# Kernel tuning notes

Hardware: AMD Instinct MI355X
Metric: run time of the kernel (lower is better)

The kernel has to match this reference:

```python
import jax, jax.numpy as jnp
import numpy as np

K_SIZE = 5  # local window size (odd, SAME padding, stride 1)


def _local_attn(x_main, x_ref, W_main, W_ref, k_size=K_SIZE):
    # 1x1 convs == per-pixel channel matmuls
    cm = jnp.einsum('bhwc,cd->bhwd', x_main, W_main)  # query  [B,H,W,C']
    cr = jnp.einsum('bhwc,cd->bhwd', x_ref, W_ref)    # keys   [B,H,W,C']
    pad = (k_size - 1) // 2
    B, H, W, C = cr.shape
    crp = jnp.pad(cr, ((0, 0), (pad, pad), (pad, pad), (0, 0)))
    # score for each of the k*k offsets: dot(query, shifted key) per pixel.
    # Avoids materializing the [B,H,W,k*k,C] patch tensor.
    scores = [
        jnp.einsum('bhwc,bhwc->bhw', cm, crp[:, i:i + H, j:j + W, :])
        for i in range(k_size) for j in range(k_size)
    ]
    # the layer concatenates the query itself as the last "key" (self score)
    scores.append(jnp.einsum('bhwc,bhwc->bhw', cm, cm))
    attn = jnp.stack(scores, axis=-1)  # [B,H,W,k*k+1]
    return jax.nn.softmax(attn, axis=-1)


def setup_inputs() -> dict:
    key = jax.random.key(0)
    k1, k2, k3, k4 = jax.random.split(key, 4)
    B, H, W, C = 4, 128, 128, 64
    Ci = 64  # intermediate_dim
    return {
        'x_main': jax.random.normal(k1, (B, H, W, C), jnp.float32),
        'x_ref': jax.random.normal(k2, (B, H, W, C), jnp.float32),
        'W_main': jax.random.normal(k3, (C, Ci), jnp.float32) * (2.0 / C) ** 0.5,
        'W_ref': jax.random.normal(k4, (C, Ci), jnp.float32) * (2.0 / C) ** 0.5,
    }


def reference(x_main, x_ref, W_main, W_ref):
    return _local_attn(x_main, x_ref, W_main, W_ref)
```

## Files before the change

### kernel.cpp

```cpp
#include <hip/hip_runtime.h>
#include <math.h>

#define HDIM 128
#define WDIM 128
#define CDIM 64
#define BDIM 4

#define TILE_W 16
#define TILE_H 8
#define HALO_W 20
#define HALO_H 12
#define NHALO (HALO_W * HALO_H)
#define PSTRIDE 68
#define WSTRIDE 65

typedef short bf16x8 __attribute__((ext_vector_type(8)));
typedef float f32x4  __attribute__((ext_vector_type(4)));

__device__ __forceinline__ void split_bf16(float f, short& hi, short& lo) {
    unsigned u = __float_as_uint(f);
    hi = (short)(u >> 16);
    float hf = __uint_as_float(u & 0xffff0000u);
    float l  = f - hf;
    lo = (short)(__float_as_uint(l) >> 16);
}

__global__ __launch_bounds__(256, 1)
void fused_mfma_local_attn(const float* __restrict__ xm,
                           const float* __restrict__ xr,
                           const float* __restrict__ Wm,
                           const float* __restrict__ Wr,
                           float* __restrict__ out) {
    __shared__ float lds[16320];
    float* Wsh = lds;
    float* cms = lds + 4352;
    float* crs = lds;

    const int t    = threadIdx.x;
    const int lane = t & 63;
    const int wv   = t >> 6;
    const int m    = lane & 15;
    const int quad = lane >> 4;
    const int tx0  = blockIdx.x * TILE_W;
    const int ty0  = blockIdx.y * TILE_H;
    const int b    = blockIdx.z;

    #pragma unroll
    for (int i = 0; i < 16; ++i) {
        int L = t + 256 * i;
        Wsh[(L >> 6) * WSTRIDE + (L & 63)] = Wm[L];
    }
    __syncthreads();

    bf16x8 Bhi[2][4], Blo[2][4];
    #pragma unroll
    for (int ks = 0; ks < 2; ++ks)
        #pragma unroll
        for (int nt = 0; nt < 4; ++nt)
            #pragma unroll
            for (int j = 0; j < 8; ++j) {
                float f = Wsh[(ks * 32 + quad * 8 + j) * WSTRIDE + nt * 16 + m];
                short hi, lo; split_bf16(f, hi, lo);
                Bhi[ks][nt][j] = hi; Blo[ks][nt][j] = lo;
            }

    #pragma unroll
    for (int s = 0; s < 2; ++s) {
        const int tile = 2 * wv + s;
        const float* ap = xm + (((size_t)b * HDIM + ty0 + tile) * WDIM
                                + tx0 + m) * CDIM + quad * 8;
        float4 p0 = *(const float4*)(ap);
        float4 p1 = *(const float4*)(ap + 4);
        float4 p2 = *(const float4*)(ap + 32);
        float4 p3 = *(const float4*)(ap + 36);

        bf16x8 Ahi[2], Alo[2];
        {
            float fv[16] = {p0.x,p0.y,p0.z,p0.w, p1.x,p1.y,p1.z,p1.w,
                            p2.x,p2.y,p2.z,p2.w, p3.x,p3.y,p3.z,p3.w};
            #pragma unroll
            for (int ks = 0; ks < 2; ++ks)
                #pragma unroll
                for (int j = 0; j < 8; ++j) {
                    short hi, lo; split_bf16(fv[8 * ks + j], hi, lo);
                    Ahi[ks][j] = hi; Alo[ks][j] = lo;
                }
        }
        f32x4 acc[4];
        #pragma unroll
        for (int nt = 0; nt < 4; ++nt)
            { acc[nt][0]=0.f; acc[nt][1]=0.f; acc[nt][2]=0.f; acc[nt][3]=0.f; }
        #pragma unroll
        for (int ks = 0; ks < 2; ++ks)
            #pragma unroll
            for (int nt = 0; nt < 4; ++nt) {
                acc[nt] = __builtin_amdgcn_mfma_f32_16x16x32_bf16(Ahi[ks], Bhi[ks][nt], acc[nt], 0,0,0);
                acc[nt] = __builtin_amdgcn_mfma_f32_16x16x32_bf16(Ahi[ks], Blo[ks][nt], acc[nt], 0,0,0);
                acc[nt] = __builtin_amdgcn_mfma_f32_16x16x32_bf16(Alo[ks], Bhi[ks][nt], acc[nt], 0,0,0);
            }
        #pragma unroll
        for (int nt = 0; nt < 4; ++nt)
            #pragma unroll
            for (int r = 0; r < 4; ++r)
                cms[(tile * 16 + quad * 4 + r) * PSTRIDE + nt * 16 + m] = acc[nt][r];
    }
    __syncthreads();

    #pragma unroll
    for (int i = 0; i < 16; ++i) {
        int L = t + 256 * i;
        Wsh[(L >> 6) * WSTRIDE + (L & 63)] = Wr[L];
    }
    __syncthreads();

    #pragma unroll
    for (int ks = 0; ks < 2; ++ks)
        #pragma unroll
        for (int nt = 0; nt < 4; ++nt)
            #pragma unroll
            for (int j = 0; j < 8; ++j) {
                float f = Wsh[(ks * 32 + quad * 8 + j) * WSTRIDE + nt * 16 + m];
                short hi, lo; split_bf16(f, hi, lo);
                Bhi[ks][nt][j] = hi; Blo[ks][nt][j] = lo;
            }

    const int pl = t >> 1;
    const int cg = t & 1;
    float4 qv[8];
    #pragma unroll
    for (int mq = 0; mq < 8; ++mq)
        qv[mq] = *(const float4*)&cms[pl * PSTRIDE + cg * 32 + 4 * mq];
    __syncthreads();

    #pragma unroll
    for (int s = 0; s < 4; ++s) {
        const int tj = wv + 4 * s;
        if (tj < 15) {
            const int hp = tj * 16 + m;
            const int hy = hp / HALO_W;
            const int hx = hp - hy * HALO_W;
            const int gy = ty0 + hy - 2, gx = tx0 + hx - 2;
            float4 p0 = make_float4(0,0,0,0), p1 = p0, p2 = p0, p3 = p0;
            if (gy >= 0 && gy < HDIM && gx >= 0 && gx < WDIM) {
                const float* ap = xr + (((size_t)b * HDIM + gy) * WDIM + gx) * CDIM
                                  + quad * 8;
                p0 = *(const float4*)(ap);
                p1 = *(const float4*)(ap + 4);
                p2 = *(const float4*)(ap + 32);
                p3 = *(const float4*)(ap + 36);
            }
            bf16x8 Ahi[2], Alo[2];
            {
                float fv[16] = {p0.x,p0.y,p0.z,p0.w, p1.x,p1.y,p1.z,p1.w,
                                p2.x,p2.y,p2.z,p2.w, p3.x,p3.y,p3.z,p3.w};
                #pragma unroll
                for (int ks = 0; ks < 2; ++ks)
                    #pragma unroll
                    for (int j = 0; j < 8; ++j) {
                        short hi, lo; split_bf16(fv[8 * ks + j], hi, lo);
                        Ahi[ks][j] = hi; Alo[ks][j] = lo;
                    }
            }
            f32x4 acc[4];
            #pragma unroll
            for (int nt = 0; nt < 4; ++nt)
                { acc[nt][0]=0.f; acc[nt][1]=0.f; acc[nt][2]=0.f; acc[nt][3]=0.f; }
            #pragma unroll
            for (int ks = 0; ks < 2; ++ks)
                #pragma unroll
                for (int nt = 0; nt < 4; ++nt) {
                    acc[nt] = __builtin_amdgcn_mfma_f32_16x16x32_bf16(Ahi[ks], Bhi[ks][nt], acc[nt], 0,0,0);
                    acc[nt] = __builtin_amdgcn_mfma_f32_16x16x32_bf16(Ahi[ks], Blo[ks][nt], acc[nt], 0,0,0);
                    acc[nt] = __builtin_amdgcn_mfma_f32_16x16x32_bf16(Alo[ks], Bhi[ks][nt], acc[nt], 0,0,0);
                }
            #pragma unroll
            for (int nt = 0; nt < 4; ++nt)
                #pragma unroll
                for (int r = 0; r < 4; ++r)
                    crs[(tj * 16 + quad * 4 + r) * PSTRIDE + nt * 16 + m] = acc[nt][r];
        }
    }
    __syncthreads();

    const int lx = pl & (TILE_W - 1);
    const int ly = pl >> 4;
    const size_t gpx = ((size_t)b * HDIM + ty0 + ly) * WDIM + tx0 + lx;

    float s[26];
    #pragma unroll
    for (int k = 0; k < 25; ++k) {
        const int i = k / 5, j = k % 5;
        const int p = (ly + i) * HALO_W + (lx + j);
        const float4* kp = (const float4*)&crs[p * PSTRIDE + cg * 32];
        float acc = 0.f;
        #pragma unroll
        for (int mq = 0; mq < 8; ++mq) {
            float4 v = kp[mq];
            acc = fmaf(qv[mq].x, v.x, acc);
            acc = fmaf(qv[mq].y, v.y, acc);
            acc = fmaf(qv[mq].z, v.z, acc);
            acc = fmaf(qv[mq].w, v.w, acc);
        }
        s[k] = acc;
    }
    {
        float acc = 0.f;
        #pragma unroll
        for (int mq = 0; mq < 8; ++mq) {
            float4 v = qv[mq];
            acc = fmaf(v.x, v.x, acc);
            acc = fmaf(v.y, v.y, acc);
            acc = fmaf(v.z, v.z, acc);
            acc = fmaf(v.w, v.w, acc);
        }
        s[25] = acc;
    }

    #pragma unroll
    for (int k = 0; k < 26; ++k) s[k] += __shfl_xor(s[k], 1);

    float mx = s[0];
    #pragma unroll
    for (int k = 1; k < 26; ++k) mx = fmaxf(mx, s[k]);
    float sum = 0.f;
    #pragma unroll
    for (int k = 0; k < 26; ++k) { s[k] = __expf(s[k] - mx); sum += s[k]; }
    const float inv = 1.f / sum;

    float* op = &out[gpx * 26 + cg * 13];
    if (cg == 0) {
        #pragma unroll
        for (int k = 0; k < 13; ++k) op[k] = s[k] * inv;
    } else {
        #pragma unroll
        for (int k = 0; k < 13; ++k) op[k] = s[13 + k] * inv;
    }
}

extern "C" void kernel_launch(void* const* d_in, const int* in_sizes, int n_in,
                              void* d_out, int out_size, void* d_ws, size_t ws_size,
                              hipStream_t stream) {
    const float* xm = (const float*)d_in[0];
    const float* xr = (const float*)d_in[1];
    const float* Wm = (const float*)d_in[2];
    const float* Wr = (const float*)d_in[3];
    float* outp = (float*)d_out;

    dim3 g(WDIM / TILE_W, HDIM / TILE_H, BDIM);
    fused_mfma_local_attn<<<g, 256, 0, stream>>>(xm, xr, Wm, Wr, outp);
}
```

Measured before the change: 89.44 us.

## Split fused kernel into projection kernel and score/softmax kernel via workspace

Splits the fused kernel into two. The first projects both x_main and x_ref to global workspace buffers using split-bf16 MFMA, with no halo recomputation. The second loads the projected key halo and the queries from the workspace and computes the 26 scores and the softmax. This removes the redundant projection of halo pixels (12x20 per 8x16 tile) and the serialized phases within one block. In exchange it adds a global round trip of about 32 MB of intermediates and a second kernel launch.

```diff
diff --git a/kernel.cpp b/kernel.cpp
--- a/kernel.cpp
+++ b/kernel.cpp
@@ -10,7 +10,7 @@
 #define TILE_H 8
 #define HALO_W 20
 #define HALO_H 12
-#define NHALO (HALO_W * HALO_H)
+#define NPX (HALO_W * HALO_H)
 #define PSTRIDE 68
 #define WSTRIDE 65
 
@@ -25,16 +25,12 @@
     lo = (short)(__float_as_uint(l) >> 16);
 }
 
+
 __global__ __launch_bounds__(256, 1)
-void fused_mfma_local_attn(const float* __restrict__ xm,
-                           const float* __restrict__ xr,
-                           const float* __restrict__ Wm,
-                           const float* __restrict__ Wr,
-                           float* __restrict__ out) {
-    __shared__ float lds[16320];
-    float* Wsh = lds;
-    float* cms = lds + 4352;
-    float* crs = lds;
+void k1_proj(const float* __restrict__ xm, const float* __restrict__ xr,
+             const float* __restrict__ Wm, const float* __restrict__ Wr,
+             float* __restrict__ cm, float* __restrict__ cr) {
+    __shared__ float Wsh[2][64 * WSTRIDE];
 
     const int t    = threadIdx.x;
     const int lane = t & 63;
@@ -48,107 +44,39 @@
     #pragma unroll
     for (int i = 0; i < 16; ++i) {
         int L = t + 256 * i;
-        Wsh[(L >> 6) * WSTRIDE + (L & 63)] = Wm[L];
+        int r = L >> 6, c = L & 63;
+        Wsh[0][r * WSTRIDE + c] = Wm[L];
+        Wsh[1][r * WSTRIDE + c] = Wr[L];
     }
     __syncthreads();
 
-    bf16x8 Bhi[2][4], Blo[2][4];
-    #pragma unroll
-    for (int ks = 0; ks < 2; ++ks)
-        #pragma unroll
-        for (int nt = 0; nt < 4; ++nt)
-            #pragma unroll
-            for (int j = 0; j < 8; ++j) {
-                float f = Wsh[(ks * 32 + quad * 8 + j) * WSTRIDE + nt * 16 + m];
-                short hi, lo; split_bf16(f, hi, lo);
-                Bhi[ks][nt][j] = hi; Blo[ks][nt][j] = lo;
-            }
-
-    #pragma unroll
-    for (int s = 0; s < 2; ++s) {
-        const int tile = 2 * wv + s;
-        const float* ap = xm + (((size_t)b * HDIM + ty0 + tile) * WDIM
-                                + tx0 + m) * CDIM + quad * 8;
-        float4 p0 = *(const float4*)(ap);
-        float4 p1 = *(const float4*)(ap + 4);
-        float4 p2 = *(const float4*)(ap + 32);
-        float4 p3 = *(const float4*)(ap + 36);
-
-        bf16x8 Ahi[2], Alo[2];
-        {
-            float fv[16] = {p0.x,p0.y,p0.z,p0.w, p1.x,p1.y,p1.z,p1.w,
-                            p2.x,p2.y,p2.z,p2.w, p3.x,p3.y,p3.z,p3.w};
-            #pragma unroll
-            for (int ks = 0; ks < 2; ++ks)
+    #pragma unroll 1
+    for (int w = 0; w < 2; ++w) {
+        const float* __restrict__ src = w ? xr : xm;
+        float* __restrict__ dst       = w ? cr : cm;
+
+        bf16x8 Bhi[2][4], Blo[2][4];
+        #pragma unroll
+        for (int ks = 0; ks < 2; ++ks)
+            #pragma unroll
+            for (int nt = 0; nt < 4; ++nt)
                 #pragma unroll
                 for (int j = 0; j < 8; ++j) {
-                    short hi, lo; split_bf16(fv[8 * ks + j], hi, lo);
-                    Ahi[ks][j] = hi; Alo[ks][j] = lo;
+                    float f = Wsh[w][(ks * 32 + quad * 8 + j) * WSTRIDE + nt * 16 + m];
+                    short hi, lo; split_bf16(f, hi, lo);
+                    Bhi[ks][nt][j] = hi; Blo[ks][nt][j] = lo;
                 }
-        }
-        f32x4 acc[4];
-        #pragma unroll
-        for (int nt = 0; nt < 4; ++nt)
-            { acc[nt][0]=0.f; acc[nt][1]=0.f; acc[nt][2]=0.f; acc[nt][3]=0.f; }
-        #pragma unroll
-        for (int ks = 0; ks < 2; ++ks)
-            #pragma unroll
-            for (int nt = 0; nt < 4; ++nt) {
-                acc[nt] = __builtin_amdgcn_mfma_f32_16x16x32_bf16(Ahi[ks], Bhi[ks][nt], acc[nt], 0,0,0);
-                acc[nt] = __builtin_amdgcn_mfma_f32_16x16x32_bf16(Ahi[ks], Blo[ks][nt], acc[nt], 0,0,0);
-                acc[nt] = __builtin_amdgcn_mfma_f32_16x16x32_bf16(Alo[ks], Bhi[ks][nt], acc[nt], 0,0,0);
-            }
-        #pragma unroll
-        for (int nt = 0; nt < 4; ++nt)
-            #pragma unroll
-            for (int r = 0; r < 4; ++r)
-                cms[(tile * 16 + quad * 4 + r) * PSTRIDE + nt * 16 + m] = acc[nt][r];
-    }
-    __syncthreads();
-
-    #pragma unroll
-    for (int i = 0; i < 16; ++i) {
-        int L = t + 256 * i;
-        Wsh[(L >> 6) * WSTRIDE + (L & 63)] = Wr[L];
-    }
-    __syncthreads();
-
-    #pragma unroll
-    for (int ks = 0; ks < 2; ++ks)
-        #pragma unroll
-        for (int nt = 0; nt < 4; ++nt)
-            #pragma unroll
-            for (int j = 0; j < 8; ++j) {
-                float f = Wsh[(ks * 32 + quad * 8 + j) * WSTRIDE + nt * 16 + m];
-                short hi, lo; split_bf16(f, hi, lo);
-                Bhi[ks][nt][j] = hi; Blo[ks][nt][j] = lo;
-            }
-
-    const int pl = t >> 1;
-    const int cg = t & 1;
-    float4 qv[8];
-    #pragma unroll
-    for (int mq = 0; mq < 8; ++mq)
-        qv[mq] = *(const float4*)&cms[pl * PSTRIDE + cg * 32 + 4 * mq];
-    __syncthreads();
-
-    #pragma unroll
-    for (int s = 0; s < 4; ++s) {
-        const int tj = wv + 4 * s;
-        if (tj < 15) {
-            const int hp = tj * 16 + m;
-            const int hy = hp / HALO_W;
-            const int hx = hp - hy * HALO_W;
-            const int gy = ty0 + hy - 2, gx = tx0 + hx - 2;
-            float4 p0 = make_float4(0,0,0,0), p1 = p0, p2 = p0, p3 = p0;
-            if (gy >= 0 && gy < HDIM && gx >= 0 && gx < WDIM) {
-                const float* ap = xr + (((size_t)b * HDIM + gy) * WDIM + gx) * CDIM
-                                  + quad * 8;
-                p0 = *(const float4*)(ap);
-                p1 = *(const float4*)(ap + 4);
-                p2 = *(const float4*)(ap + 32);
-                p3 = *(const float4*)(ap + 36);
-            }
+
+        #pragma unroll
+        for (int s = 0; s < 2; ++s) {
+            const int tile = 2 * wv + s;
+            const float* ap = src + (((size_t)b * HDIM + ty0 + tile) * WDIM
+                                     + tx0 + m) * CDIM + quad * 8;
+            float4 p0 = *(const float4*)(ap);
+            float4 p1 = *(const float4*)(ap + 4);
+            float4 p2 = *(const float4*)(ap + 32);
+            float4 p3 = *(const float4*)(ap + 36);
+
             bf16x8 Ahi[2], Alo[2];
             {
                 float fv[16] = {p0.x,p0.y,p0.z,p0.w, p1.x,p1.y,p1.z,p1.w,
@@ -177,14 +105,44 @@
             for (int nt = 0; nt < 4; ++nt)
                 #pragma unroll
                 for (int r = 0; r < 4; ++r)
-                    crs[(tj * 16 + quad * 4 + r) * PSTRIDE + nt * 16 + m] = acc[nt][r];
+                    dst[(((size_t)b * HDIM + ty0 + tile) * WDIM
+                         + tx0 + quad * 4 + r) * CDIM + nt * 16 + m] = acc[nt][r];
         }
     }
-    __syncthreads();
-
+}
+
+__global__ __launch_bounds__(256, 1)
+void k2_scores(const float* __restrict__ cm, const float* __restrict__ cr,
+               float* __restrict__ out) {
+    __shared__ float crs[NPX * PSTRIDE];
+
+    const int t   = threadIdx.x;
+    const int tx0 = blockIdx.x * TILE_W;
+    const int ty0 = blockIdx.y * TILE_H;
+    const int b   = blockIdx.z;
+
+    #pragma unroll
+    for (int i = 0; i < 15; ++i) {
+        int L  = t + 256 * i;
+        int p  = L >> 4, sl = L & 15;
+        int hy = p / HALO_W, hx = p - hy * HALO_W;
+        int gy = ty0 + hy - 2, gx = tx0 + hx - 2;
+        float4 v = make_float4(0.f, 0.f, 0.f, 0.f);
+        if (gy >= 0 && gy < HDIM && gx >= 0 && gx < WDIM)
+            v = *(const float4*)&cr[(((size_t)b * HDIM + gy) * WDIM + gx) * CDIM + sl * 4];
+        *(float4*)&crs[p * PSTRIDE + sl * 4] = v;
+    }
+
+    const int pl = t >> 1;
+    const int cg = t & 1;
     const int lx = pl & (TILE_W - 1);
     const int ly = pl >> 4;
     const size_t gpx = ((size_t)b * HDIM + ty0 + ly) * WDIM + tx0 + lx;
+    float4 qv[8];
+    #pragma unroll
+    for (int mq = 0; mq < 8; ++mq)
+        qv[mq] = *(const float4*)&cm[gpx * CDIM + cg * 32 + 4 * mq];
+    __syncthreads();
 
     float s[26];
     #pragma unroll
@@ -246,6 +204,10 @@
     const float* Wr = (const float*)d_in[3];
     float* outp = (float*)d_out;
 
+    float* cmw = (float*)d_ws;
+    float* crw = cmw + (size_t)BDIM * HDIM * WDIM * CDIM;
+
     dim3 g(WDIM / TILE_W, HDIM / TILE_H, BDIM);
-    fused_mfma_local_attn<<<g, 256, 0, stream>>>(xm, xr, Wm, Wr, outp);
-}
+    k1_proj<<<g, 256, 0, stream>>>(xm, xr, Wm, Wr, cmw, crw);
+    k2_scores<<<g, 256, 0, stream>>>(cmw, crw, outp);
+}
```

After: 98.58 us. +10.2%, slower.
